# Kernel tuning notes

Hardware: AMD Instinct MI355X
Metric: run time of the kernel (lower is better)

Reference implementation:

```python
import jax, jax.numpy as jnp
import numpy as np
import math

B, C, H, W = 4, 256, 64, 64
HID = 32  # max(C//8, 32)

def setup_inputs() -> dict:
    key = jax.random.key(0)
    ks = jax.random.split(key, 7)
    x = jax.random.normal(ks[0], (B, C, H, W), dtype=jnp.float32)
    # 1x1 conv weights stored as [out, in]
    w_ce1 = jax.random.normal(ks[1], (HID, C), dtype=jnp.float32) * math.sqrt(2.0 / HID)
    w_ce2 = jax.random.normal(ks[2], (1, HID), dtype=jnp.float32) * math.sqrt(2.0)
    xav = math.sqrt(6.0 / (C + C))
    wq = jax.random.uniform(ks[3], (C, C), jnp.float32, -xav, xav)
    wk = jax.random.uniform(ks[4], (C, C), jnp.float32, -xav, xav)
    wv = jax.random.uniform(ks[5], (C, C), jnp.float32, -xav, xav)
    wproj = jax.random.uniform(ks[6], (C, C), jnp.float32, -xav, xav)
    return {"x": x, "w_ce1": w_ce1, "w_ce2": w_ce2, "wq": wq, "wk": wk, "wv": wv, "wproj": wproj}

def reference(x, w_ce1, w_ce2, wq, wk, wv, wproj):
    b, c, h, w = x.shape
    n = h * w
    # complexity gate: global avg+max pool -> 1x1 convs -> sigmoid, shape [B,1,1,1]
    feat = jnp.mean(x, axis=(2, 3)) + jnp.max(x, axis=(2, 3))       # [B,C]
    hid = jax.nn.silu(jnp.einsum('oc,bc->bo', w_ce1, feat))          # [B,HID]
    complexity = jax.nn.sigmoid(jnp.einsum('oh,bh->bo', w_ce2, hid)) # [B,1]
    complexity = complexity[:, :, None, None]                        # [B,1,1,1]
    # qkv via 1x1 convs, flattened to tokens
    xf = x.reshape(b, c, n)                                          # [B,C,N]
    q = jnp.einsum('oc,bcn->bno', wq, xf)                            # [B,N,C]
    k = jnp.einsum('oc,bcn->bon', wk, xf)                            # [B,C,N]
    v = jnp.einsum('oc,bcn->bno', wv, xf)                            # [B,N,C]
    attn = jax.nn.softmax(jnp.einsum('bnc,bcm->bnm', q, k) * (1.0 / math.sqrt(c)), axis=-1)
    x_attn = jnp.einsum('bnm,bmc->bnc', attn, v)                     # [B,N,C]
    x_attn = x_attn.transpose(0, 2, 1).reshape(b, c, h, w)           # [B,C,H,W]
    proj = jnp.einsum('oc,bchw->bohw', wproj, x_attn)
    return x + proj * complexity
```

## Files before the change

### kernel.cpp

```cpp
#include <hip/hip_runtime.h>
#include <hip/hip_bf16.h>

#define B_ 4
#define C_ 256
#define N_ 4096
#define BN_ (B_*N_)

typedef float f32x4 __attribute__((ext_vector_type(4)));
typedef short bf16x8 __attribute__((ext_vector_type(8)));
typedef short short4v __attribute__((ext_vector_type(4)));
typedef int   int4v  __attribute__((ext_vector_type(4)));

static __device__ __forceinline__ short f2bf(float f){
  unsigned u = __builtin_bit_cast(unsigned, f);
  u += 0x7FFFu + ((u >> 16) & 1u);
  return (short)(u >> 16);
}
static __device__ __forceinline__ float bf2f(short s){
  unsigned u = ((unsigned)(unsigned short)s) << 16;
  return __builtin_bit_cast(float, u);
}
static __device__ __forceinline__ int cvtpk(float lo, float hi){
  int r;
  asm("v_cvt_pk_bf16_f32 %0, %1, %2" : "=v"(r) : "v"(lo), "v"(hi));
  return r;
}
static __device__ __forceinline__ void gload_lds16(const void* g, void* l){
  __builtin_amdgcn_global_load_lds((const __attribute__((address_space(1))) unsigned*)g,
                                   (__attribute__((address_space(3))) unsigned*)l, 16, 0, 0);
}

__global__ __launch_bounds__(256) void k_feat(const float* __restrict__ x, float* __restrict__ feat){
  int row = blockIdx.x;
  const f32x4* p = (const f32x4*)(x + (size_t)row * N_);
  float s = 0.f, mx = -1e30f;
  for (int i = threadIdx.x; i < N_/4; i += 256){
    f32x4 v = p[i];
    s += v.x + v.y + v.z + v.w;
    mx = fmaxf(mx, fmaxf(fmaxf(v.x, v.y), fmaxf(v.z, v.w)));
  }
  __shared__ float ss[256];
  __shared__ float sm[256];
  int t = threadIdx.x;
  ss[t] = s; sm[t] = mx;
  __syncthreads();
  for (int off = 128; off > 0; off >>= 1){
    if (t < off){ ss[t] += ss[t+off]; sm[t] = fmaxf(sm[t], sm[t+off]); }
    __syncthreads();
  }
  if (t == 0) feat[row] = ss[0] * (1.f/(float)N_) + sm[0];
}

__global__ __launch_bounds__(64) void k_cplx(const float* __restrict__ feat, const float* __restrict__ w1,
    const float* __restrict__ w2, float* __restrict__ cplx){
  int b = blockIdx.x, l = threadIdx.x;
  float contrib = 0.f;
  if (l < 32){
    const float* wr = w1 + l*C_;
    const float* f = feat + b*C_;
    float d = 0.f;
    for (int c = 0; c < C_; c++) d += wr[c]*f[c];
    float sg = 1.f/(1.f + expf(-d));
    contrib = (d*sg)*w2[l];
  }
  #pragma unroll
  for (int off = 1; off < 64; off <<= 1) contrib += __shfl_xor(contrib, off);
  if (l == 0) cplx[b] = 1.f/(1.f + expf(-contrib));
}

__global__ __launch_bounds__(256) void k_wcvt(const float* __restrict__ a, const float* __restrict__ b,
    const float* __restrict__ c, const float* __restrict__ d,
    short* __restrict__ oa, short* __restrict__ ob2, short* __restrict__ oc, short* __restrict__ od){
  int m = blockIdx.x >> 6;
  int off = (blockIdx.x & 63)*1024 + threadIdx.x*4;
  const float* src = (m==0)?a:(m==1)?b:(m==2)?c:d;
  short* dst = (m==0)?oa:(m==1)?ob2:(m==2)?oc:od;
  f32x4 v = *(const f32x4*)(src + off);
  short4v s;
  #pragma unroll
  for (int j = 0; j < 4; j++) s[j] = f2bf(v[j]);
  *(short4v*)(dst + off) = s;
}

__global__ __launch_bounds__(256) void k_qkv(const float* __restrict__ x,
    const short* __restrict__ wqb, const short* __restrict__ wkb, const short* __restrict__ wvb,
    short* __restrict__ Q, short* __restrict__ K, short* __restrict__ Vt){
  int b = blockIdx.z, o0 = blockIdx.y*64, n0 = blockIdx.x*64;
  int tid = threadIdx.x, w = tid>>6, l = tid&63, lq = l&15, lg = l>>4;
  const float* xb = x + (size_t)b*C_*N_;
  int nrow = n0 + w*16 + lq;
  f32x4 zero = {0.f,0.f,0.f,0.f};
  f32x4 acc[3][4];
  #pragma unroll
  for (int m = 0; m < 3; m++)
    #pragma unroll
    for (int s = 0; s < 4; s++) acc[m][s] = zero;

  for (int kk = 0; kk < 8; ++kk){
    int c0 = kk*32 + lg*8;
    bf16x8 a;
    #pragma unroll
    for (int j = 0; j < 8; j++) a[j] = f2bf(xb[(size_t)(c0+j)*N_ + nrow]);
    #pragma unroll
    for (int s = 0; s < 4; s++){
      int base = (o0 + s*16 + lq)*C_ + c0;
      bf16x8 aq = *(const bf16x8*)(wqb + base);
      bf16x8 ak = *(const bf16x8*)(wkb + base);
      bf16x8 av = *(const bf16x8*)(wvb + base);
      acc[0][s] = __builtin_amdgcn_mfma_f32_16x16x32_bf16(a, aq, acc[0][s], 0, 0, 0);
      acc[1][s] = __builtin_amdgcn_mfma_f32_16x16x32_bf16(a, ak, acc[1][s], 0, 0, 0);
      acc[2][s] = __builtin_amdgcn_mfma_f32_16x16x32_bf16(a, av, acc[2][s], 0, 0, 0);
    }
  }
  #pragma unroll
  for (int s = 0; s < 4; s++)
    #pragma unroll
    for (int r = 0; r < 4; r++){
      int n = n0 + w*16 + lg*4 + r;
      int o = o0 + s*16 + lq;
      size_t idx = ((size_t)b*N_ + n)*C_ + o;
      Q[idx] = f2bf(acc[0][s][r] * 0.0625f);
      K[idx] = f2bf(acc[1][s][r]);
    }
  __shared__ short lv[64][72];
  #pragma unroll
  for (int s = 0; s < 4; s++)
    #pragma unroll
    for (int r = 0; r < 4; r++)
      lv[s*16 + lq][w*16 + lg*4 + r] = f2bf(acc[2][s][r]);
  __syncthreads();
  #pragma unroll
  for (int i = 0; i < 16; i++){
    int orow = i*4 + (tid>>6);
    int ncol = tid & 63;
    Vt[((size_t)b*C_ + o0 + orow)*N_ + n0 + ncol] = lv[orow][ncol];
  }
}

__global__ __launch_bounds__(512, 2) void k_attn4(const short* __restrict__ Q, const short* __restrict__ K,
    const short* __restrict__ Vt, short* __restrict__ Op, float* __restrict__ Mp, float* __restrict__ Lp){
  extern __shared__ short smem[];
  short* KsBase = smem;
  short* VsBase = smem + 16384;

  int bid = blockIdx.x;
  int xcd = bid & 7, idx = bid >> 3;
  int b = xcd >> 1;
  int part = ((xcd & 1) << 1) | (idx & 1);
  int n0 = (idx >> 1) * 256;
  int kv0 = part * 1024;
  int tid = threadIdx.x, w = tid>>6, l = tid&63, lq = l&15, lg = l>>4;
  const short* Qb = Q + (size_t)b*N_*C_;
  const short* Kb = K + (size_t)b*N_*C_;
  const short* Vb = Vt + (size_t)b*C_*N_;

  int cid0 = w*128 + l;
  auto stage = [&](int buf, int m0){
    short* kd = KsBase + buf*8192 + w*1024;
    short* vd = VsBase + buf*8192 + w*1024;
    #pragma unroll
    for (int i = 0; i < 2; i++){
      int cid = cid0 + i*64;
      int krow = cid >> 5;
      int kch  = (cid & 31) ^ (krow & 7);
      gload_lds16(Kb + (size_t)(m0 + krow)*C_ + kch*8, kd + i*512);
      int vrow = cid >> 2;
      int vch  = (cid & 3) ^ (vrow & 3);
      gload_lds16(Vb + (size_t)vrow*N_ + m0 + vch*8, vd + i*512);
    }
  };

  bf16x8 qf[2][8];
  #pragma unroll
  for (int qt = 0; qt < 2; qt++){
    const short* qrow = Qb + (size_t)(n0 + w*32 + qt*16 + lq)*C_ + lg*8;
    #pragma unroll
    for (int kk = 0; kk < 8; kk++) qf[qt][kk] = *(const bf16x8*)(qrow + kk*32);
  }

  f32x4 zero = {0.f,0.f,0.f,0.f};
  f32x4 oacc[2][16];
  #pragma unroll
  for (int qt = 0; qt < 2; qt++)
    #pragma unroll
    for (int c = 0; c < 16; c++) oacc[qt][c] = zero;
  float m[2] = {-1e30f, -1e30f}, lsum[2] = {0.f, 0.f};
  int swz = lq & 7;
  int a01 = ((2*(lg & 1))*16 + lq) * 4;
  int a23 = a01 + 64;
  bool hiHalf = (l >= 32);

  stage(0, kv0);
  __syncthreads();
  int cur = 0;

  for (int mt = 0; mt < 32; mt++){
    if (mt + 1 < 32) stage(cur^1, kv0 + (mt+1)*32);
    const short* Kc = KsBase + cur*8192;
    const short* Vc = VsBase + cur*8192;

    f32x4 sa[2][2];
    #pragma unroll
    for (int qt = 0; qt < 2; qt++){ sa[qt][0] = zero; sa[qt][1] = zero; }
    __builtin_amdgcn_s_setprio(1);
    #pragma unroll
    for (int s = 0; s < 2; s++){
      const short* krowp = Kc + (s*16 + lq)*256;
      #pragma unroll
      for (int kk = 0; kk < 8; kk++){
        bf16x8 kf = *(const bf16x8*)(krowp + (((kk*4 + lg) ^ swz) << 3));
        sa[0][s] = __builtin_amdgcn_mfma_f32_16x16x32_bf16(kf, qf[0][kk], sa[0][s], 0, 0, 0);
        sa[1][s] = __builtin_amdgcn_mfma_f32_16x16x32_bf16(kf, qf[1][kk], sa[1][s], 0, 0, 0);
      }
    }
    __builtin_amdgcn_s_setprio(0);

    int W[2][2][2];
    #pragma unroll
    for (int qt = 0; qt < 2; qt++){
      float pmax = sa[qt][0][0];
      #pragma unroll
      for (int s = 0; s < 2; s++)
        #pragma unroll
        for (int r = 0; r < 4; r++) pmax = fmaxf(pmax, sa[qt][s][r]);
      pmax = fmaxf(pmax, __shfl_xor(pmax, 16));
      pmax = fmaxf(pmax, __shfl_xor(pmax, 32));
      if (__any(pmax > m[qt] + 8.f)){
        float mn = fmaxf(m[qt], pmax);
        float al = __expf(m[qt] - mn);
        m[qt] = mn;
        lsum[qt] *= al;
        float alo[4];
        #pragma unroll
        for (int r = 0; r < 4; r++) alo[r] = __shfl(al, (l & 48) | (lg*4 + r));
        #pragma unroll
        for (int c = 0; c < 16; c++){
          f32x4 o = oacc[qt][c];
          o[0]*=alo[0]; o[1]*=alo[1]; o[2]*=alo[2]; o[3]*=alo[3];
          oacc[qt][c] = o;
        }
      }
      #pragma unroll
      for (int s = 0; s < 2; s++)
        #pragma unroll
        for (int r = 0; r < 4; r++) sa[qt][s][r] = __expf(sa[qt][s][r] - m[qt]);
      float ts = 0.f;
      #pragma unroll
      for (int s = 0; s < 2; s++) ts += sa[qt][s][0] + sa[qt][s][1] + sa[qt][s][2] + sa[qt][s][3];
      ts += __shfl_xor(ts, 16);
      ts += __shfl_xor(ts, 32);
      lsum[qt] += ts;
      #pragma unroll
      for (int s = 0; s < 2; s++){
        W[qt][s][0] = cvtpk(sa[qt][s][0], sa[qt][s][1]);
        W[qt][s][1] = cvtpk(sa[qt][s][2], sa[qt][s][3]);
      }
    }

    bf16x8 pa[2];
    #pragma unroll
    for (int qt = 0; qt < 2; qt++){
      int lo0 = __builtin_amdgcn_ds_bpermute(a01, W[qt][0][0]);
      int hi0 = __builtin_amdgcn_ds_bpermute(a01, W[qt][1][0]);
      int lo1 = __builtin_amdgcn_ds_bpermute(a01, W[qt][0][1]);
      int hi1 = __builtin_amdgcn_ds_bpermute(a01, W[qt][1][1]);
      int lo2 = __builtin_amdgcn_ds_bpermute(a23, W[qt][0][0]);
      int hi2 = __builtin_amdgcn_ds_bpermute(a23, W[qt][1][0]);
      int lo3 = __builtin_amdgcn_ds_bpermute(a23, W[qt][0][1]);
      int hi3 = __builtin_amdgcn_ds_bpermute(a23, W[qt][1][1]);
      int4v pw;
      pw[0] = hiHalf ? hi0 : lo0;
      pw[1] = hiHalf ? hi1 : lo1;
      pw[2] = hiHalf ? hi2 : lo2;
      pw[3] = hiHalf ? hi3 : lo3;
      pa[qt] = __builtin_bit_cast(bf16x8, pw);
    }

    __builtin_amdgcn_s_setprio(1);
    #pragma unroll
    for (int c = 0; c < 16; c++){
      int vr = c*16 + lq;
      bf16x8 vbf = *(const bf16x8*)(Vc + vr*32 + ((lg ^ (vr & 3)) << 3));
      oacc[0][c] = __builtin_amdgcn_mfma_f32_16x16x32_bf16(pa[0], vbf, oacc[0][c], 0, 0, 0);
      oacc[1][c] = __builtin_amdgcn_mfma_f32_16x16x32_bf16(pa[1], vbf, oacc[1][c], 0, 0, 0);
    }
    __builtin_amdgcn_s_setprio(0);

    __syncthreads();
    cur ^= 1;
  }

  #pragma unroll
  for (int qt = 0; qt < 2; qt++){
    float inv = 1.f / lsum[qt];
    float invo[4];
    #pragma unroll
    for (int r = 0; r < 4; r++) invo[r] = __shfl(inv, (l & 48) | (lg*4 + r));
    #pragma unroll
    for (int c = 0; c < 16; c++)
      #pragma unroll
      for (int r = 0; r < 4; r++){
        int n = n0 + w*32 + qt*16 + lg*4 + r;
        Op[((size_t)part*BN_ + (size_t)b*N_ + n)*C_ + c*16 + lq] = f2bf(oacc[qt][c][r]*invo[r]);
      }
    if (lg == 0){
      int n = n0 + w*32 + qt*16 + lq;
      Mp[part*BN_ + b*N_ + n] = m[qt];
      Lp[part*BN_ + b*N_ + n] = lsum[qt];
    }
  }
}

__global__ __launch_bounds__(256) void k_comb4(const short* __restrict__ Op, const float* __restrict__ Mp,
    const float* __restrict__ Lp, short* __restrict__ Xa){
  int tid = threadIdx.x;
  int rg = blockIdx.x*8 + (tid>>5);
  int cc = (tid&31)*8;
  float mv[4], lv[4];
  float m = -1e30f;
  #pragma unroll
  for (int p = 0; p < 4; p++){ mv[p] = Mp[p*BN_ + rg]; lv[p] = Lp[p*BN_ + rg]; m = fmaxf(m, mv[p]); }
  float wgt[4], wsum = 0.f;
  #pragma unroll
  for (int p = 0; p < 4; p++){ wgt[p] = lv[p]*__expf(mv[p]-m); wsum += wgt[p]; }
  float inv = 1.f/wsum;
  float acc[8];
  #pragma unroll
  for (int j = 0; j < 8; j++) acc[j] = 0.f;
  #pragma unroll
  for (int p = 0; p < 4; p++){
    bf16x8 o = *(const bf16x8*)(Op + ((size_t)p*BN_ + rg)*C_ + cc);
    #pragma unroll
    for (int j = 0; j < 8; j++) acc[j] += wgt[p]*bf2f(o[j]);
  }
  bf16x8 r;
  #pragma unroll
  for (int j = 0; j < 8; j++) r[j] = f2bf(acc[j]*inv);
  *(bf16x8*)(Xa + (size_t)rg*C_ + cc) = r;
}

__global__ __launch_bounds__(512) void k_attn2(const short* __restrict__ Q, const short* __restrict__ K,
    const short* __restrict__ Vt, short* __restrict__ Op, float* __restrict__ Mp, float* __restrict__ Lp){
  extern __shared__ short smem[];
  short* Ks = smem;
  short* Vs = smem + 32768;
  int bid = blockIdx.x;
  int xcd = bid & 7;
  int b = xcd >> 1;
  int half = xcd & 1;
  int n0 = (bid >> 3) * 128;
  int kv0 = half * 2048;
  int tid = threadIdx.x, w = tid>>6, l = tid&63, lq = l&15, lg = l>>4;
  const short* Qb = Q + (size_t)b*N_*C_;
  const short* Kb = K + (size_t)b*N_*C_;
  const short* Vb = Vt + (size_t)b*C_*N_;
  short* lp = smem + 65536 + w*(16*72);
  int krow0 = w*8 + (l>>5);
  int kchunk0 = l&31;
  int vrow0 = w*32 + (l>>3);
  int vchunk = (l&7) ^ ((l>>3)&7);
  bf16x8 qf[8];
  {
    const short* qrow = Qb + (size_t)(n0 + w*16 + lq)*C_ + lg*8;
    #pragma unroll
    for (int kk = 0; kk < 8; kk++) qf[kk] = *(const bf16x8*)(qrow + kk*32);
  }
  f32x4 zero = {0.f,0.f,0.f,0.f};
  f32x4 oacc[16];
  #pragma unroll
  for (int c = 0; c < 16; c++) oacc[c] = zero;
  float mrow[4], lsum[4];
  #pragma unroll
  for (int r = 0; r < 4; r++){ mrow[r] = -1e30f; lsum[r] = 0.f; }
  int swz = lq & 7;
  auto stage = [&](int buf, int m0){
    short* kd = Ks + buf*16384 + w*2048;
    short* vd = Vs + buf*16384 + w*2048;
    #pragma unroll
    for (int i = 0; i < 4; i++){
      int row = krow0 + i*2;
      int chunk = kchunk0 ^ (row & 7);
      gload_lds16(Kb + (size_t)(m0 + row)*C_ + chunk*8, kd + i*512);
    }
    #pragma unroll
    for (int i = 0; i < 4; i++){
      int row = vrow0 + i*8;
      gload_lds16(Vb + (size_t)row*N_ + m0 + vchunk*8, vd + i*512);
    }
  };
  stage(0, kv0);
  __syncthreads();
  int cur = 0;
  for (int mt = 0; mt < 32; mt++){
    if (mt + 1 < 32) stage(cur^1, kv0 + (mt+1)*64);
    const short* Kc = Ks + cur*16384;
    const short* Vc = Vs + cur*16384;
    f32x4 sa[4];
    #pragma unroll
    for (int s = 0; s < 4; s++) sa[s] = zero;
    __builtin_amdgcn_s_setprio(1);
    #pragma unroll
    for (int s = 0; s < 4; s++){
      const short* krowp = Kc + (s*16 + lq)*256;
      #pragma unroll
      for (int kk = 0; kk < 8; kk++){
        bf16x8 kf = *(const bf16x8*)(krowp + (((kk*4 + lg) ^ swz) << 3));
        sa[s] = __builtin_amdgcn_mfma_f32_16x16x32_bf16(qf[kk], kf, sa[s], 0, 0, 0);
      }
    }
    __builtin_amdgcn_s_setprio(0);
    float tmax[4];
    #pragma unroll
    for (int r = 0; r < 4; r++){
      float t = fmaxf(fmaxf(sa[0][r], sa[1][r]), fmaxf(sa[2][r], sa[3][r]));
      t = fmaxf(t, __shfl_xor(t, 1));
      t = fmaxf(t, __shfl_xor(t, 2));
      t = fmaxf(t, __shfl_xor(t, 4));
      t = fmaxf(t, __shfl_xor(t, 8));
      tmax[r] = t;
    }
    bool need = (tmax[0] > mrow[0]+8.f) | (tmax[1] > mrow[1]+8.f) |
                (tmax[2] > mrow[2]+8.f) | (tmax[3] > mrow[3]+8.f);
    if (__any(need)){
      float al[4];
      #pragma unroll
      for (int r = 0; r < 4; r++){
        float mn = fmaxf(mrow[r], tmax[r]);
        al[r] = __expf(mrow[r] - mn);
        mrow[r] = mn;
        lsum[r] *= al[r];
      }
      #pragma unroll
      for (int c = 0; c < 16; c++){
        f32x4 o = oacc[c];
        o[0]*=al[0]; o[1]*=al[1]; o[2]*=al[2]; o[3]*=al[3];
        oacc[c] = o;
      }
    }
    #pragma unroll
    for (int s = 0; s < 4; s++)
      #pragma unroll
      for (int r = 0; r < 4; r++)
        sa[s][r] = __expf(sa[s][r] - mrow[r]);
    #pragma unroll
    for (int r = 0; r < 4; r++){
      float t = sa[0][r] + sa[1][r] + sa[2][r] + sa[3][r];
      t += __shfl_xor(t, 1); t += __shfl_xor(t, 2);
      t += __shfl_xor(t, 4); t += __shfl_xor(t, 8);
      lsum[r] += t;
    }
    #pragma unroll
    for (int s = 0; s < 4; s++)
      #pragma unroll
      for (int r = 0; r < 4; r++)
        lp[(lg*4 + r)*72 + s*16 + lq] = f2bf(sa[s][r]);
    __builtin_amdgcn_sched_barrier(0);
    __builtin_amdgcn_s_setprio(1);
    #pragma unroll
    for (int s2 = 0; s2 < 2; s2++){
      bf16x8 pa = *(const bf16x8*)(lp + lq*72 + s2*32 + lg*8);
      #pragma unroll
      for (int c = 0; c < 16; c++){
        bf16x8 vbf = *(const bf16x8*)(Vc + (c*16 + lq)*64 + (((s2*4 + lg) ^ swz) << 3));
        oacc[c] = __builtin_amdgcn_mfma_f32_16x16x32_bf16(pa, vbf, oacc[c], 0, 0, 0);
      }
    }
    __builtin_amdgcn_s_setprio(0);
    __builtin_amdgcn_sched_barrier(0);
    __syncthreads();
    cur ^= 1;
  }
  float inv[4];
  #pragma unroll
  for (int r = 0; r < 4; r++) inv[r] = 1.f / lsum[r];
  #pragma unroll
  for (int c = 0; c < 16; c++)
    #pragma unroll
    for (int r = 0; r < 4; r++){
      int n = n0 + w*16 + lg*4 + r;
      Op[((size_t)half*BN_ + (size_t)b*N_ + n)*C_ + c*16 + lq] = f2bf(oacc[c][r]*inv[r]);
    }
  if (lq == 0){
    #pragma unroll
    for (int r = 0; r < 4; r++){
      int n = n0 + w*16 + lg*4 + r;
      Mp[half*BN_ + b*N_ + n] = mrow[r];
      Lp[half*BN_ + b*N_ + n] = lsum[r];
    }
  }
}

__global__ __launch_bounds__(256) void k_comb2(const short* __restrict__ Op, const float* __restrict__ Mp,
    const float* __restrict__ Lp, short* __restrict__ Xa){
  int tid = threadIdx.x;
  int rg = blockIdx.x*8 + (tid>>5);
  int cc = (tid&31)*8;
  float m1 = Mp[rg], m2 = Mp[BN_ + rg];
  float l1 = Lp[rg], l2 = Lp[BN_ + rg];
  float m = fmaxf(m1, m2);
  float w1 = l1 * __expf(m1 - m);
  float w2 = l2 * __expf(m2 - m);
  float inv = 1.f/(w1 + w2);
  w1 *= inv; w2 *= inv;
  bf16x8 o1 = *(const bf16x8*)(Op + (size_t)rg*C_ + cc);
  bf16x8 o2 = *(const bf16x8*)(Op + ((size_t)BN_ + rg)*C_ + cc);
  bf16x8 r;
  #pragma unroll
  for (int j = 0; j < 8; j++){
    float f = w1*bf2f(o1[j]) + w2*bf2f(o2[j]);
    r[j] = f2bf(f);
  }
  *(bf16x8*)(Xa + (size_t)rg*C_ + cc) = r;
}

__global__ __launch_bounds__(256) void k_proj(const float* __restrict__ x, const short* __restrict__ wpb,
    const short* __restrict__ Xa, const float* __restrict__ cplx, float* __restrict__ out){
  int b = blockIdx.z, o0 = blockIdx.y*64, n0 = blockIdx.x*64;
  int tid = threadIdx.x, w = tid>>6, l = tid&63, lq = l&15, lg = l>>4;
  f32x4 zero = {0.f,0.f,0.f,0.f};
  f32x4 acc[4];
  #pragma unroll
  for (int s = 0; s < 4; s++) acc[s] = zero;
  int orow = o0 + w*16 + lq;
  for (int kk = 0; kk < 8; kk++){
    int c0 = kk*32 + lg*8;
    bf16x8 aw = *(const bf16x8*)(wpb + orow*C_ + c0);
    #pragma unroll
    for (int s = 0; s < 4; s++){
      bf16x8 xb = *(const bf16x8*)(Xa + ((size_t)b*N_ + n0 + s*16 + lq)*C_ + c0);
      acc[s] = __builtin_amdgcn_mfma_f32_16x16x32_bf16(aw, xb, acc[s], 0, 0, 0);
    }
  }
  float cp = cplx[b];
  #pragma unroll
  for (int s = 0; s < 4; s++)
    #pragma unroll
    for (int r = 0; r < 4; r++){
      int o = o0 + w*16 + lg*4 + r;
      int n = n0 + s*16 + lq;
      size_t idx = ((size_t)b*C_ + o)*N_ + n;
      out[idx] = x[idx] + cp*acc[s][r];
    }
}

extern "C" void kernel_launch(void* const* d_in, const int* in_sizes, int n_in,
                              void* d_out, int out_size, void* d_ws, size_t ws_size,
                              hipStream_t stream){
  const float* x     = (const float*)d_in[0];
  const float* w_ce1 = (const float*)d_in[1];
  const float* w_ce2 = (const float*)d_in[2];
  const float* wq    = (const float*)d_in[3];
  const float* wk    = (const float*)d_in[4];
  const float* wv    = (const float*)d_in[5];
  const float* wproj = (const float*)d_in[6];
  float* out = (float*)d_out;

  const size_t mat = (size_t)B_*N_*C_;
  const size_t needA = (3*mat + 4*mat + 4*(size_t)C_*C_)*2 + (8*(size_t)BN_ + B_*C_ + 16)*4;
  bool use4 = ws_size >= needA;
  int nparts = use4 ? 4 : 2;

  char* p = (char*)d_ws;
  short* Q   = (short*)p;            p += mat*2;
  short* K   = (short*)p;            p += mat*2;
  short* Vt  = (short*)p;            p += mat*2;
  short* Op  = (short*)p;            p += (size_t)nparts*mat*2;
  float* Mp  = (float*)p;            p += (size_t)nparts*BN_*4;
  float* Lp  = (float*)p;            p += (size_t)nparts*BN_*4;
  float* feat= (float*)p;            p += B_*C_*4;
  float* cplx= (float*)p;            p += 64;
  short* wqb = (short*)p;            p += (size_t)C_*C_*2;
  short* wkb = (short*)p;            p += (size_t)C_*C_*2;
  short* wvb = (short*)p;            p += (size_t)C_*C_*2;
  short* wpb = (short*)p;
  short* Xa  = Q;

  const int SMEM_A4 = 65536;
  const int SMEM_A2 = (16384*2 + 16384*2 + 8*16*72) * 2;
  hipFuncSetAttribute((const void*)k_attn4, hipFuncAttributeMaxDynamicSharedMemorySize, SMEM_A4);
  hipFuncSetAttribute((const void*)k_attn2, hipFuncAttributeMaxDynamicSharedMemorySize, SMEM_A2);

  hipLaunchKernelGGL(k_feat, dim3(B_*C_), dim3(256), 0, stream, x, feat);
  hipLaunchKernelGGL(k_cplx, dim3(B_), dim3(64), 0, stream, feat, w_ce1, w_ce2, cplx);
  hipLaunchKernelGGL(k_wcvt, dim3(256), dim3(256), 0, stream, wq, wk, wv, wproj, wqb, wkb, wvb, wpb);
  hipLaunchKernelGGL(k_qkv, dim3(64,4,4), dim3(256), 0, stream, x, wqb, wkb, wvb, Q, K, Vt);
  if (use4){
    hipLaunchKernelGGL(k_attn4, dim3(256), dim3(512), SMEM_A4, stream, Q, K, Vt, Op, Mp, Lp);
    hipLaunchKernelGGL(k_comb4, dim3(BN_/8), dim3(256), 0, stream, Op, Mp, Lp, Xa);
  } else {
    hipLaunchKernelGGL(k_attn2, dim3(256), dim3(512), SMEM_A2, stream, Q, K, Vt, Op, Mp, Lp);
    hipLaunchKernelGGL(k_comb2, dim3(BN_/8), dim3(256), 0, stream, Op, Mp, Lp, Xa);
  }
  hipLaunchKernelGGL(k_proj, dim3(64,4,4), dim3(256), 0, stream, x, wpb, Xa, cplx, out);
}
```

Before: 175.4 us.

## Compute transposed PV with 16x16x16 MFMA to drop P bpermute shuffles

Reworks the P·V stage so the softmax probabilities are used directly in their score-MFMA register layout as the B operand of 16x16x16 bf16 MFMAs, computing O transposed. This removes the eight ds_bpermute shuffles per tile and the per-row alpha/inv broadcasts, and lets the output be written as contiguous 4-element bf16 stores. The V LDS swizzle changes to match the new read pattern. The trade-off is twice as many MFMA instructions, each on half-width operands, and smaller LDS reads.

```diff
diff --git a/kernel.cpp b/kernel.cpp
--- a/kernel.cpp
+++ b/kernel.cpp
@@ -8,8 +8,9 @@
 
 typedef float f32x4 __attribute__((ext_vector_type(4)));
 typedef short bf16x8 __attribute__((ext_vector_type(8)));
+typedef short bf16x4 __attribute__((ext_vector_type(4)));
 typedef short short4v __attribute__((ext_vector_type(4)));
-typedef int   int4v  __attribute__((ext_vector_type(4)));
+typedef int   int2v  __attribute__((ext_vector_type(2)));
 
 static __device__ __forceinline__ short f2bf(float f){
   unsigned u = __builtin_bit_cast(unsigned, f);
@@ -29,6 +30,19 @@
   __builtin_amdgcn_global_load_lds((const __attribute__((address_space(1))) unsigned*)g,
                                    (__attribute__((address_space(3))) unsigned*)l, 16, 0, 0);
 }
+
+#if __has_builtin(__builtin_amdgcn_mfma_f32_16x16x16bf16_1k)
+static __device__ __forceinline__ f32x4 mfma16(bf16x4 a, bf16x4 b, f32x4 c){
+  return __builtin_amdgcn_mfma_f32_16x16x16bf16_1k(a, b, c, 0, 0, 0);
+}
+#else
+static __device__ __forceinline__ f32x4 mfma16(bf16x4 a, bf16x4 b, f32x4 c){
+  f32x4 d;
+  asm volatile("v_mfma_f32_16x16x16_bf16 %0, %1, %2, %3\n\ts_nop 7"
+               : "=v"(d) : "v"(a), "v"(b), "v"(c));
+  return d;
+}
+#endif
 
 __global__ __launch_bounds__(256) void k_feat(const float* __restrict__ x, float* __restrict__ feat){
   int row = blockIdx.x;
@@ -165,7 +179,7 @@
       int kch  = (cid & 31) ^ (krow & 7);
       gload_lds16(Kb + (size_t)(m0 + krow)*C_ + kch*8, kd + i*512);
       int vrow = cid >> 2;
-      int vch  = (cid & 3) ^ (vrow & 3);
+      int vch  = (cid & 3) ^ ((vrow >> 1) & 3);
       gload_lds16(Vb + (size_t)vrow*N_ + m0 + vch*8, vd + i*512);
     }
   };
@@ -186,9 +200,7 @@
     for (int c = 0; c < 16; c++) oacc[qt][c] = zero;
   float m[2] = {-1e30f, -1e30f}, lsum[2] = {0.f, 0.f};
   int swz = lq & 7;
-  int a01 = ((2*(lg & 1))*16 + lq) * 4;
-  int a23 = a01 + 64;
-  bool hiHalf = (l >= 32);
+  int vrot = (lq >> 1) & 3;
 
   stage(0, kv0);
   __syncthreads();
@@ -215,7 +227,7 @@
     }
     __builtin_amdgcn_s_setprio(0);
 
-    int W[2][2][2];
+    bf16x4 pb[2][2];
     #pragma unroll
     for (int qt = 0; qt < 2; qt++){
       float pmax = sa[qt][0][0];
@@ -230,13 +242,10 @@
         float al = __expf(m[qt] - mn);
         m[qt] = mn;
         lsum[qt] *= al;
-        float alo[4];
-        #pragma unroll
-        for (int r = 0; r < 4; r++) alo[r] = __shfl(al, (l & 48) | (lg*4 + r));
         #pragma unroll
         for (int c = 0; c < 16; c++){
           f32x4 o = oacc[qt][c];
-          o[0]*=alo[0]; o[1]*=alo[1]; o[2]*=alo[2]; o[3]*=alo[3];
+          o[0]*=al; o[1]*=al; o[2]*=al; o[3]*=al;
           oacc[qt][c] = o;
         }
       }
@@ -252,37 +261,25 @@
       lsum[qt] += ts;
       #pragma unroll
       for (int s = 0; s < 2; s++){
-        W[qt][s][0] = cvtpk(sa[qt][s][0], sa[qt][s][1]);
-        W[qt][s][1] = cvtpk(sa[qt][s][2], sa[qt][s][3]);
-      }
-    }
-
-    bf16x8 pa[2];
-    #pragma unroll
-    for (int qt = 0; qt < 2; qt++){
-      int lo0 = __builtin_amdgcn_ds_bpermute(a01, W[qt][0][0]);
-      int hi0 = __builtin_amdgcn_ds_bpermute(a01, W[qt][1][0]);
-      int lo1 = __builtin_amdgcn_ds_bpermute(a01, W[qt][0][1]);
-      int hi1 = __builtin_amdgcn_ds_bpermute(a01, W[qt][1][1]);
-      int lo2 = __builtin_amdgcn_ds_bpermute(a23, W[qt][0][0]);
-      int hi2 = __builtin_amdgcn_ds_bpermute(a23, W[qt][1][0]);
-      int lo3 = __builtin_amdgcn_ds_bpermute(a23, W[qt][0][1]);
-      int hi3 = __builtin_amdgcn_ds_bpermute(a23, W[qt][1][1]);
-      int4v pw;
-      pw[0] = hiHalf ? hi0 : lo0;
-      pw[1] = hiHalf ? hi1 : lo1;
-      pw[2] = hiHalf ? hi2 : lo2;
-      pw[3] = hiHalf ? hi3 : lo3;
-      pa[qt] = __builtin_bit_cast(bf16x8, pw);
+        int2v t;
+        t[0] = cvtpk(sa[qt][s][0], sa[qt][s][1]);
+        t[1] = cvtpk(sa[qt][s][2], sa[qt][s][3]);
+        pb[qt][s] = __builtin_bit_cast(bf16x4, t);
+      }
     }
 
     __builtin_amdgcn_s_setprio(1);
     #pragma unroll
-    for (int c = 0; c < 16; c++){
-      int vr = c*16 + lq;
-      bf16x8 vbf = *(const bf16x8*)(Vc + vr*32 + ((lg ^ (vr & 3)) << 3));
-      oacc[0][c] = __builtin_amdgcn_mfma_f32_16x16x32_bf16(pa[0], vbf, oacc[0][c], 0, 0, 0);
-      oacc[1][c] = __builtin_amdgcn_mfma_f32_16x16x32_bf16(pa[1], vbf, oacc[1][c], 0, 0, 0);
+    for (int ct = 0; ct < 16; ct++){
+      int vr = ct*16 + lq;
+      const short* vrow = Vc + vr*32;
+      #pragma unroll
+      for (int s = 0; s < 2; s++){
+        int p16 = (2*s + (lg>>1)) ^ vrot;
+        bf16x4 va = *(const bf16x4*)(vrow + p16*8 + (lg&1)*4);
+        oacc[0][ct] = mfma16(va, pb[0][s], oacc[0][ct]);
+        oacc[1][ct] = mfma16(va, pb[1][s], oacc[1][ct]);
+      }
     }
     __builtin_amdgcn_s_setprio(0);
 
@@ -293,18 +290,16 @@
   #pragma unroll
   for (int qt = 0; qt < 2; qt++){
     float inv = 1.f / lsum[qt];
-    float invo[4];
-    #pragma unroll
-    for (int r = 0; r < 4; r++) invo[r] = __shfl(inv, (l & 48) | (lg*4 + r));
-    #pragma unroll
-    for (int c = 0; c < 16; c++)
-      #pragma unroll
-      for (int r = 0; r < 4; r++){
-        int n = n0 + w*32 + qt*16 + lg*4 + r;
-        Op[((size_t)part*BN_ + (size_t)b*N_ + n)*C_ + c*16 + lq] = f2bf(oacc[qt][c][r]*invo[r]);
-      }
+    int n = n0 + w*32 + qt*16 + lq;
+    short* orow = Op + ((size_t)part*BN_ + (size_t)b*N_ + n)*C_ + lg*4;
+    #pragma unroll
+    for (int ct = 0; ct < 16; ct++){
+      short4v o4;
+      #pragma unroll
+      for (int r = 0; r < 4; r++) o4[r] = f2bf(oacc[qt][ct][r]*inv);
+      *(short4v*)(orow + ct*16) = o4;
+    }
     if (lg == 0){
-      int n = n0 + w*32 + qt*16 + lq;
       Mp[part*BN_ + b*N_ + n] = m[qt];
       Lp[part*BN_ + b*N_ + n] = lsum[qt];
     }
```

Measured after the change: 185.8 us. 5.9% more time.

## Retile QKV projection so each block reads x once for all outputs

Applied to the files above, without the earlier changes.

Each QKV block now covers 16 tokens and all 256 output channels (one wave per 64-channel slice), so x is read and converted to bf16 only once per token instead of once for each of four output-channel tiles. The x fragments are preloaded into registers before the MFMA loop. The V transpose goes through a reshaped shared buffer and is written with 4-wide vector stores. In exchange, all four waves load the same x fragments redundantly, register use rises with eight preloaded bf16x8 fragments, and the Vt rows written per block are short 16-element segments.

```diff
diff --git a/kernel.cpp b/kernel.cpp
--- a/kernel.cpp
+++ b/kernel.cpp
@@ -85,10 +85,19 @@
 __global__ __launch_bounds__(256) void k_qkv(const float* __restrict__ x,
     const short* __restrict__ wqb, const short* __restrict__ wkb, const short* __restrict__ wvb,
     short* __restrict__ Q, short* __restrict__ K, short* __restrict__ Vt){
-  int b = blockIdx.z, o0 = blockIdx.y*64, n0 = blockIdx.x*64;
+  int b = blockIdx.y, n0 = blockIdx.x*16;
   int tid = threadIdx.x, w = tid>>6, l = tid&63, lq = l&15, lg = l>>4;
   const float* xb = x + (size_t)b*C_*N_;
-  int nrow = n0 + w*16 + lq;
+  int nrow = n0 + lq;
+
+  bf16x8 a[8];
+  #pragma unroll
+  for (int kk = 0; kk < 8; kk++){
+    int c0 = kk*32 + lg*8;
+    #pragma unroll
+    for (int j = 0; j < 8; j++) a[kk][j] = f2bf(xb[(size_t)(c0+j)*N_ + nrow]);
+  }
+
   f32x4 zero = {0.f,0.f,0.f,0.f};
   f32x4 acc[3][4];
   #pragma unroll
@@ -97,43 +106,44 @@
     for (int s = 0; s < 4; s++) acc[m][s] = zero;
 
   for (int kk = 0; kk < 8; ++kk){
-    int c0 = kk*32 + lg*8;
-    bf16x8 a;
-    #pragma unroll
-    for (int j = 0; j < 8; j++) a[j] = f2bf(xb[(size_t)(c0+j)*N_ + nrow]);
     #pragma unroll
     for (int s = 0; s < 4; s++){
-      int base = (o0 + s*16 + lq)*C_ + c0;
+      int base = (w*64 + s*16 + lq)*C_ + kk*32 + lg*8;
       bf16x8 aq = *(const bf16x8*)(wqb + base);
       bf16x8 ak = *(const bf16x8*)(wkb + base);
       bf16x8 av = *(const bf16x8*)(wvb + base);
-      acc[0][s] = __builtin_amdgcn_mfma_f32_16x16x32_bf16(a, aq, acc[0][s], 0, 0, 0);
-      acc[1][s] = __builtin_amdgcn_mfma_f32_16x16x32_bf16(a, ak, acc[1][s], 0, 0, 0);
-      acc[2][s] = __builtin_amdgcn_mfma_f32_16x16x32_bf16(a, av, acc[2][s], 0, 0, 0);
+      acc[0][s] = __builtin_amdgcn_mfma_f32_16x16x32_bf16(a[kk], aq, acc[0][s], 0, 0, 0);
+      acc[1][s] = __builtin_amdgcn_mfma_f32_16x16x32_bf16(a[kk], ak, acc[1][s], 0, 0, 0);
+      acc[2][s] = __builtin_amdgcn_mfma_f32_16x16x32_bf16(a[kk], av, acc[2][s], 0, 0, 0);
     }
   }
   #pragma unroll
   for (int s = 0; s < 4; s++)
     #pragma unroll
     for (int r = 0; r < 4; r++){
-      int n = n0 + w*16 + lg*4 + r;
-      int o = o0 + s*16 + lq;
+      int n = n0 + lg*4 + r;
+      int o = w*64 + s*16 + lq;
       size_t idx = ((size_t)b*N_ + n)*C_ + o;
       Q[idx] = f2bf(acc[0][s][r] * 0.0625f);
       K[idx] = f2bf(acc[1][s][r]);
     }
-  __shared__ short lv[64][72];
+  __shared__ short lv[256][18];
   #pragma unroll
   for (int s = 0; s < 4; s++)
     #pragma unroll
     for (int r = 0; r < 4; r++)
-      lv[s*16 + lq][w*16 + lg*4 + r] = f2bf(acc[2][s][r]);
+      lv[w*64 + s*16 + lq][lg*4 + r] = f2bf(acc[2][s][r]);
   __syncthreads();
-  #pragma unroll
-  for (int i = 0; i < 16; i++){
-    int orow = i*4 + (tid>>6);
-    int ncol = tid & 63;
-    Vt[((size_t)b*C_ + o0 + orow)*N_ + n0 + ncol] = lv[orow][ncol];
+  {
+    int o = tid;
+    short* dst = Vt + ((size_t)b*C_ + o)*N_ + n0;
+    #pragma unroll
+    for (int q = 0; q < 4; q++){
+      short4v v;
+      #pragma unroll
+      for (int j = 0; j < 4; j++) v[j] = lv[o][q*4 + j];
+      *(short4v*)(dst + q*4) = v;
+    }
   }
 }
 
@@ -583,7 +593,7 @@
   hipLaunchKernelGGL(k_feat, dim3(B_*C_), dim3(256), 0, stream, x, feat);
   hipLaunchKernelGGL(k_cplx, dim3(B_), dim3(64), 0, stream, feat, w_ce1, w_ce2, cplx);
   hipLaunchKernelGGL(k_wcvt, dim3(256), dim3(256), 0, stream, wq, wk, wv, wproj, wqb, wkb, wvb, wpb);
-  hipLaunchKernelGGL(k_qkv, dim3(64,4,4), dim3(256), 0, stream, x, wqb, wkb, wvb, Q, K, Vt);
+  hipLaunchKernelGGL(k_qkv, dim3(256,4), dim3(256), 0, stream, x, wqb, wkb, wvb, Q, K, Vt);
   if (use4){
     hipLaunchKernelGGL(k_attn4, dim3(256), dim3(512), SMEM_A4, stream, Q, K, Vt, Op, Mp, Lp);
     hipLaunchKernelGGL(k_comb4, dim3(BN_/8), dim3(256), 0, stream, Op, Mp, Lp, Xa);
```

Measured after the change: 257.0 us. 1.47x slower.
